# Performance work log

Measured on AMD Instinct MI355X. Metric: run time of the kernel, lower is better.

The kernel has to match this reference:

```python
import jax, jax.numpy as jnp
import numpy as np

EPS = 1e-5


def setup_inputs() -> dict:
    key = jax.random.key(0)
    ks = jax.random.split(key, 12)
    B, C, D, H, W = 16, 32, 32, 64, 64
    HID, OUT = 256, 128
    inp = {
        "x": jax.random.normal(ks[0], (B, C, D, H, W), dtype=jnp.float32),
        "bn_gamma": jax.random.normal(ks[1], (C,), dtype=jnp.float32) * 0.1 + 1.0,
        "bn_beta": jax.random.normal(ks[2], (C,), dtype=jnp.float32) * 0.1,
        "w_ih": jax.random.normal(ks[3], (HID, C), dtype=jnp.float32) / np.sqrt(C),
        "b_ih": jax.random.normal(ks[4], (HID,), dtype=jnp.float32) * 0.01,
        "w_hh": jax.random.normal(ks[5], (HID, HID), dtype=jnp.float32) / np.sqrt(HID),
        "b_hh": jax.random.normal(ks[6], (HID,), dtype=jnp.float32) * 0.01,
        "w_out": jax.random.normal(ks[7], (OUT, HID), dtype=jnp.float32) / np.sqrt(HID),
        "b_out": jax.random.normal(ks[8], (OUT,), dtype=jnp.float32) * 0.01,
        "ln_gamma": jnp.ones((OUT,), dtype=jnp.float32),
        "ln_beta": jnp.zeros((OUT,), dtype=jnp.float32),
        "pooled_depth": 8,
    }
    return inp


def reference(x, bn_gamma, bn_beta, w_ih, b_ih, w_hh, b_hh, w_out, b_out, ln_gamma, ln_beta, pooled_depth):
    B, C, D, H, W = x.shape
    P = pooled_depth
    # SyncBatchNorm (training mode: batch statistics over B, D, H, W per channel)
    mean = jnp.mean(x, axis=(0, 2, 3, 4), keepdims=True)
    var = jnp.mean((x - mean) ** 2, axis=(0, 2, 3, 4), keepdims=True)  # biased var
    g = bn_gamma.reshape(1, C, 1, 1, 1)
    b = bn_beta.reshape(1, C, 1, 1, 1)
    x = (x - mean) * jax.lax.rsqrt(var + EPS) * g + b
    x = jax.nn.relu(x)
    # AdaptiveMaxPool3d -> (P, 1, 1); D divisible by P so bins are uniform
    x = x.reshape(B, C, P, D // P, H, W).max(axis=(3, 4, 5))  # (B, C, P)
    x = jnp.transpose(x, (2, 0, 1))  # (P, B, C) -- time-major
    # RNNCell (relu) scan over time
    hx0 = jnp.zeros((B, w_hh.shape[0]), dtype=x.dtype)

    def step(hx, xt):
        hx = jax.nn.relu(xt @ w_ih.T + b_ih + hx @ w_hh.T + b_hh)
        return hx, None

    hx, _ = jax.lax.scan(step, hx0, x)
    # Output projection + LayerNorm
    out = hx @ w_out.T + b_out  # (B, OUT)
    mu = jnp.mean(out, axis=-1, keepdims=True)
    v = jnp.mean((out - mu) ** 2, axis=-1, keepdims=True)
    out = (out - mu) * jax.lax.rsqrt(v + EPS) * ln_gamma + ln_beta
    return out
```

## Files before the change

### kernel.cpp

```cpp
#include <hip/hip_runtime.h>
#include <math.h>

#define EPS 1e-5f

constexpr int Bc = 16, Cc = 32, Dc = 32, Hc = 64, Wc = 64;
constexpr int Pc = 8, HIDc = 256, OUTc = 128;
constexpr int NBINS = Bc * Cc * Pc;
constexpr float NPC_INV = 1.0f / (float)(Bc * Dc * Hc * Wc);


__global__ __launch_bounds__(256) void k1_stats(const float* __restrict__ x,
                                                float* __restrict__ ws) {
    const int bid = blockIdx.x;
    const int t = threadIdx.x;
    const float4* px = reinterpret_cast<const float4*>(x) + ((size_t)bid << 12);

    float vmax = -INFINITY, vmin = INFINITY, s = 0.f, ss = 0.f;
#pragma unroll
    for (int j = 0; j < 16; ++j) {
        float4 v = px[j * 256 + t];
        vmax = fmaxf(vmax, fmaxf(fmaxf(v.x, v.y), fmaxf(v.z, v.w)));
        vmin = fminf(vmin, fminf(fminf(v.x, v.y), fminf(v.z, v.w)));
        s += (v.x + v.y) + (v.z + v.w);
        ss = fmaf(v.x, v.x, ss); ss = fmaf(v.y, v.y, ss);
        ss = fmaf(v.z, v.z, ss); ss = fmaf(v.w, v.w, ss);
    }
#pragma unroll
    for (int off = 1; off < 64; off <<= 1) {
        vmax = fmaxf(vmax, __shfl_xor(vmax, off));
        vmin = fminf(vmin, __shfl_xor(vmin, off));
        s += __shfl_xor(s, off);
        ss += __shfl_xor(ss, off);
    }
    __shared__ float r[4][4];
    const int wid = t >> 6;
    if ((t & 63) == 0) { r[wid][0] = vmax; r[wid][1] = vmin; r[wid][2] = s; r[wid][3] = ss; }
    __syncthreads();
    if (t == 0) {
        vmax = fmaxf(fmaxf(r[0][0], r[1][0]), fmaxf(r[2][0], r[3][0]));
        vmin = fminf(fminf(r[0][1], r[1][1]), fminf(r[2][1], r[3][1]));
        s  = (r[0][2] + r[1][2]) + (r[2][2] + r[3][2]);
        ss = (r[0][3] + r[1][3]) + (r[2][3] + r[3][3]);
        ws[bid]             = vmax;
        ws[NBINS + bid]     = vmin;
        ws[2 * NBINS + bid] = s;
        ws[3 * NBINS + bid] = ss;
    }
}

__global__ __launch_bounds__(256) void k2_rnn(const float* __restrict__ ws,
                                              const float* __restrict__ bn_gamma,
                                              const float* __restrict__ bn_beta,
                                              const float* __restrict__ w_ih,
                                              const float* __restrict__ b_ih,
                                              const float* __restrict__ w_hh,
                                              const float* __restrict__ b_hh,
                                              const float* __restrict__ w_out,
                                              const float* __restrict__ b_out,
                                              const float* __restrict__ ln_gamma,
                                              const float* __restrict__ ln_beta,
                                              float* __restrict__ out) {
    const int b = blockIdx.x;
    const int t = threadIdx.x;

    __shared__ float scale_s[Cc], shift_s[Cc];
    __shared__ __align__(16) float pooled[Pc][Cc];
    __shared__ __align__(16) float u[Pc][HIDc];
    __shared__ __align__(16) float hx[2][HIDc];
    __shared__ __align__(16) float o[OUTc];
    __shared__ float red2[2];

    {
        const int c = t >> 3, r = t & 7;
        float s = 0.f, ss = 0.f;
        for (int j = 0; j < 16; ++j) {
            const int i = r + 8 * j;
            const int bid = ((i >> 3) * Cc + c) * Pc + (i & 7);
            s  += ws[2 * NBINS + bid];
            ss += ws[3 * NBINS + bid];
        }
#pragma unroll
        for (int off = 1; off < 8; off <<= 1) {
            s  += __shfl_xor(s, off);
            ss += __shfl_xor(ss, off);
        }
        if (r == 0) {
            const float mean = s * NPC_INV;
            const float var  = ss * NPC_INV - mean * mean;
            const float sc   = bn_gamma[c] * rsqrtf(var + EPS);
            scale_s[c] = sc;
            shift_s[c] = bn_beta[c] - mean * sc;
        }
    }
    __syncthreads();

    {
        const int p = t >> 5, c = t & 31;
        const int bid = (b * Cc + c) * Pc + p;
        const float sc = scale_s[c];
        const float xm = (sc >= 0.f) ? ws[bid] : ws[NBINS + bid];
        pooled[p][c] = fmaxf(fmaf(sc, xm, shift_s[c]), 0.f);
    }
    __syncthreads();

    {
        const float4* wi = reinterpret_cast<const float4*>(w_ih) + t * (Cc / 4);
        float4 wiv[8];
#pragma unroll
        for (int q = 0; q < 8; ++q) wiv[q] = wi[q];
        const float bias = b_ih[t] + b_hh[t];
#pragma unroll
        for (int p = 0; p < Pc; ++p) {
            const float4* pl = reinterpret_cast<const float4*>(&pooled[p][0]);
            float a0 = bias, a1 = 0.f, a2 = 0.f, a3 = 0.f;
#pragma unroll
            for (int q = 0; q < 8; ++q) {
                float4 pv = pl[q];
                a0 = fmaf(pv.x, wiv[q].x, a0);
                a1 = fmaf(pv.y, wiv[q].y, a1);
                a2 = fmaf(pv.z, wiv[q].z, a2);
                a3 = fmaf(pv.w, wiv[q].w, a3);
            }
            u[p][t] = (a0 + a1) + (a2 + a3);
        }
        hx[0][t] = fmaxf(u[0][t], 0.f);
    }
    __syncthreads();

    int cur = 0;
    const float4* wrow = reinterpret_cast<const float4*>(w_hh) + t * (HIDc / 4);
    for (int step = 1; step < Pc; ++step) {
        const float4* hv4 = reinterpret_cast<const float4*>(&hx[cur][0]);
        float a0 = u[step][t], a1 = 0.f, a2 = 0.f, a3 = 0.f;
#pragma unroll
        for (int k4 = 0; k4 < HIDc / 4; ++k4) {
            float4 wv = wrow[k4];
            float4 hv = hv4[k4];
            a0 = fmaf(hv.x, wv.x, a0);
            a1 = fmaf(hv.y, wv.y, a1);
            a2 = fmaf(hv.z, wv.z, a2);
            a3 = fmaf(hv.w, wv.w, a3);
        }
        hx[cur ^ 1][t] = fmaxf((a0 + a1) + (a2 + a3), 0.f);
        __syncthreads();
        cur ^= 1;
    }

    if (t < OUTc) {
        const float4* wo = reinterpret_cast<const float4*>(w_out) + t * (HIDc / 4);
        const float4* hv4 = reinterpret_cast<const float4*>(&hx[cur][0]);
        float a0 = b_out[t], a1 = 0.f, a2 = 0.f, a3 = 0.f;
#pragma unroll
        for (int k4 = 0; k4 < HIDc / 4; ++k4) {
            float4 wv = wo[k4];
            float4 hv = hv4[k4];
            a0 = fmaf(hv.x, wv.x, a0);
            a1 = fmaf(hv.y, wv.y, a1);
            a2 = fmaf(hv.z, wv.z, a2);
            a3 = fmaf(hv.w, wv.w, a3);
        }
        o[t] = (a0 + a1) + (a2 + a3);
    }
    __syncthreads();
    if (t < 64) {
        const float x0 = o[t], x1 = o[t + 64];
        float s = x0 + x1, ss = x0 * x0 + x1 * x1;
#pragma unroll
        for (int off = 1; off < 64; off <<= 1) {
            s  += __shfl_xor(s, off);
            ss += __shfl_xor(ss, off);
        }
        if (t == 0) { red2[0] = s; red2[1] = ss; }
    }
    __syncthreads();
    if (t < OUTc) {
        const float mu  = red2[0] * (1.0f / OUTc);
        const float var = red2[1] * (1.0f / OUTc) - mu * mu;
        const float rs  = rsqrtf(var + EPS);
        out[b * OUTc + t] = (o[t] - mu) * rs * ln_gamma[t] + ln_beta[t];
    }
}

extern "C" void kernel_launch(void* const* d_in, const int* in_sizes, int n_in,
                              void* d_out, int out_size, void* d_ws, size_t ws_size,
                              hipStream_t stream) {
    const float* x        = (const float*)d_in[0];
    const float* bn_gamma = (const float*)d_in[1];
    const float* bn_beta  = (const float*)d_in[2];
    const float* w_ih     = (const float*)d_in[3];
    const float* b_ih     = (const float*)d_in[4];
    const float* w_hh     = (const float*)d_in[5];
    const float* b_hh     = (const float*)d_in[6];
    const float* w_out    = (const float*)d_in[7];
    const float* b_out    = (const float*)d_in[8];
    const float* ln_gamma = (const float*)d_in[9];
    const float* ln_beta  = (const float*)d_in[10];
    float* out = (float*)d_out;
    float* ws  = (float*)d_ws;

    k1_stats<<<NBINS, 256, 0, stream>>>(x, ws);
    k2_rnn<<<Bc, 256, 0, stream>>>(ws, bn_gamma, bn_beta, w_ih, b_ih, w_hh, b_hh,
                                   w_out, b_out, ln_gamma, ln_beta, out);
}
```

Before: 68.71 us.

## Split RNN recurrence across 1024 threads with register-resident w_hh slices

The RNN kernel grows from 256 to 1024 threads per batch block. Each hidden unit's dot product is split into four K-segments whose partial sums are reduced through shared memory, and each thread keeps its w_hh slice in registers across all timesteps. The output projection is likewise split four ways with a shuffle reduction, and the BN stat reduction uses wider lanes. This shortens the serial latency of the small second kernel but adds an extra barrier per step and more register pressure, while the dominant stats kernel is unchanged.

```diff
diff --git a/kernel.cpp b/kernel.cpp
--- a/kernel.cpp
+++ b/kernel.cpp
@@ -48,39 +48,43 @@
     }
 }
 
-__global__ __launch_bounds__(256) void k2_rnn(const float* __restrict__ ws,
-                                              const float* __restrict__ bn_gamma,
-                                              const float* __restrict__ bn_beta,
-                                              const float* __restrict__ w_ih,
-                                              const float* __restrict__ b_ih,
-                                              const float* __restrict__ w_hh,
-                                              const float* __restrict__ b_hh,
-                                              const float* __restrict__ w_out,
-                                              const float* __restrict__ b_out,
-                                              const float* __restrict__ ln_gamma,
-                                              const float* __restrict__ ln_beta,
-                                              float* __restrict__ out) {
+__global__ __launch_bounds__(1024) void k2_rnn(const float* __restrict__ ws,
+                                               const float* __restrict__ bn_gamma,
+                                               const float* __restrict__ bn_beta,
+                                               const float* __restrict__ w_ih,
+                                               const float* __restrict__ b_ih,
+                                               const float* __restrict__ w_hh,
+                                               const float* __restrict__ b_hh,
+                                               const float* __restrict__ w_out,
+                                               const float* __restrict__ b_out,
+                                               const float* __restrict__ ln_gamma,
+                                               const float* __restrict__ ln_beta,
+                                               float* __restrict__ out) {
     const int b = blockIdx.x;
     const int t = threadIdx.x;
+    const int h = t & 255;
+    const int q = t >> 8;
 
     __shared__ float scale_s[Cc], shift_s[Cc];
     __shared__ __align__(16) float pooled[Pc][Cc];
     __shared__ __align__(16) float u[Pc][HIDc];
-    __shared__ __align__(16) float hx[2][HIDc];
+    __shared__ __align__(16) float hx[HIDc];
+    __shared__ __align__(16) float part[4][HIDc];
     __shared__ __align__(16) float o[OUTc];
     __shared__ float red2[2];
 
     {
-        const int c = t >> 3, r = t & 7;
+        const int c = t >> 5, r = t & 31;
         float s = 0.f, ss = 0.f;
-        for (int j = 0; j < 16; ++j) {
-            const int i = r + 8 * j;
+#pragma unroll
+        for (int j = 0; j < 4; ++j) {
+            const int i = r + 32 * j;
             const int bid = ((i >> 3) * Cc + c) * Pc + (i & 7);
             s  += ws[2 * NBINS + bid];
             ss += ws[3 * NBINS + bid];
         }
 #pragma unroll
-        for (int off = 1; off < 8; off <<= 1) {
+        for (int off = 1; off < 32; off <<= 1) {
             s  += __shfl_xor(s, off);
             ss += __shfl_xor(ss, off);
         }
@@ -94,7 +98,7 @@
     }
     __syncthreads();
 
-    {
+    if (t < Pc * Cc) {
         const int p = t >> 5, c = t & 31;
         const int bid = (b * Cc + c) * Pc + p;
         const float sc = scale_s[c];
@@ -104,64 +108,81 @@
     __syncthreads();
 
     {
-        const float4* wi = reinterpret_cast<const float4*>(w_ih) + t * (Cc / 4);
+        const float4* wi = reinterpret_cast<const float4*>(w_ih) + h * (Cc / 4);
         float4 wiv[8];
 #pragma unroll
-        for (int q = 0; q < 8; ++q) wiv[q] = wi[q];
-        const float bias = b_ih[t] + b_hh[t];
-#pragma unroll
-        for (int p = 0; p < Pc; ++p) {
+        for (int e = 0; e < 8; ++e) wiv[e] = wi[e];
+        const float bias = b_ih[h] + b_hh[h];
+#pragma unroll
+        for (int pp = 0; pp < 2; ++pp) {
+            const int p = q + 4 * pp;
             const float4* pl = reinterpret_cast<const float4*>(&pooled[p][0]);
             float a0 = bias, a1 = 0.f, a2 = 0.f, a3 = 0.f;
 #pragma unroll
-            for (int q = 0; q < 8; ++q) {
-                float4 pv = pl[q];
-                a0 = fmaf(pv.x, wiv[q].x, a0);
-                a1 = fmaf(pv.y, wiv[q].y, a1);
-                a2 = fmaf(pv.z, wiv[q].z, a2);
-                a3 = fmaf(pv.w, wiv[q].w, a3);
+            for (int e = 0; e < 8; ++e) {
+                float4 pv = pl[e];
+                a0 = fmaf(pv.x, wiv[e].x, a0);
+                a1 = fmaf(pv.y, wiv[e].y, a1);
+                a2 = fmaf(pv.z, wiv[e].z, a2);
+                a3 = fmaf(pv.w, wiv[e].w, a3);
             }
-            u[p][t] = (a0 + a1) + (a2 + a3);
-        }
-        hx[0][t] = fmaxf(u[0][t], 0.f);
-    }
-    __syncthreads();
-
-    int cur = 0;
-    const float4* wrow = reinterpret_cast<const float4*>(w_hh) + t * (HIDc / 4);
+            u[p][h] = (a0 + a1) + (a2 + a3);
+        }
+    }
+
+    float4 wreg[16];
+    {
+        const float4* wr = reinterpret_cast<const float4*>(w_hh) + h * (HIDc / 4) + q * 16;
+#pragma unroll
+        for (int e = 0; e < 16; ++e) wreg[e] = wr[e];
+    }
+    __syncthreads();
+
+    if (t < HIDc) hx[t] = fmaxf(u[0][t], 0.f);
+    __syncthreads();
+
     for (int step = 1; step < Pc; ++step) {
-        const float4* hv4 = reinterpret_cast<const float4*>(&hx[cur][0]);
-        float a0 = u[step][t], a1 = 0.f, a2 = 0.f, a3 = 0.f;
-#pragma unroll
-        for (int k4 = 0; k4 < HIDc / 4; ++k4) {
-            float4 wv = wrow[k4];
-            float4 hv = hv4[k4];
+        const float4* hv4 = reinterpret_cast<const float4*>(&hx[q * 64]);
+        float a0 = 0.f, a1 = 0.f, a2 = 0.f, a3 = 0.f;
+#pragma unroll
+        for (int e = 0; e < 16; ++e) {
+            float4 wv = wreg[e];
+            float4 hv = hv4[e];
             a0 = fmaf(hv.x, wv.x, a0);
             a1 = fmaf(hv.y, wv.y, a1);
             a2 = fmaf(hv.z, wv.z, a2);
             a3 = fmaf(hv.w, wv.w, a3);
         }
-        hx[cur ^ 1][t] = fmaxf((a0 + a1) + (a2 + a3), 0.f);
+        part[q][h] = (a0 + a1) + (a2 + a3);
         __syncthreads();
-        cur ^= 1;
-    }
-
-    if (t < OUTc) {
-        const float4* wo = reinterpret_cast<const float4*>(w_out) + t * (HIDc / 4);
-        const float4* hv4 = reinterpret_cast<const float4*>(&hx[cur][0]);
-        float a0 = b_out[t], a1 = 0.f, a2 = 0.f, a3 = 0.f;
-#pragma unroll
-        for (int k4 = 0; k4 < HIDc / 4; ++k4) {
-            float4 wv = wo[k4];
-            float4 hv = hv4[k4];
+        if (q == 0) {
+            const float v = u[step][h] + ((part[0][h] + part[1][h]) + (part[2][h] + part[3][h]));
+            hx[h] = fmaxf(v, 0.f);
+        }
+        __syncthreads();
+    }
+
+    if (t < 4 * OUTc) {
+        const int oi = t >> 2, seg = t & 3;
+        const float4* wo = reinterpret_cast<const float4*>(w_out) + oi * (HIDc / 4) + seg * 16;
+        const float4* hv4 = reinterpret_cast<const float4*>(&hx[seg * 64]);
+        float a0 = (seg == 0) ? b_out[oi] : 0.f, a1 = 0.f, a2 = 0.f, a3 = 0.f;
+#pragma unroll
+        for (int e = 0; e < 16; ++e) {
+            float4 wv = wo[e];
+            float4 hv = hv4[e];
             a0 = fmaf(hv.x, wv.x, a0);
             a1 = fmaf(hv.y, wv.y, a1);
             a2 = fmaf(hv.z, wv.z, a2);
             a3 = fmaf(hv.w, wv.w, a3);
         }
-        o[t] = (a0 + a1) + (a2 + a3);
-    }
-    __syncthreads();
+        float s = (a0 + a1) + (a2 + a3);
+        s += __shfl_xor(s, 1);
+        s += __shfl_xor(s, 2);
+        if (seg == 0) o[oi] = s;
+    }
+    __syncthreads();
+
     if (t < 64) {
         const float x0 = o[t], x1 = o[t + 64];
         float s = x0 + x1, ss = x0 * x0 + x1 * x1;
@@ -199,6 +220,6 @@
     float* ws  = (float*)d_ws;
 
     k1_stats<<<NBINS, 256, 0, stream>>>(x, ws);
-    k2_rnn<<<Bc, 256, 0, stream>>>(ws, bn_gamma, bn_beta, w_ih, b_ih, w_hh, b_hh,
-                                   w_out, b_out, ln_gamma, ln_beta, out);
+    k2_rnn<<<Bc, 1024, 0, stream>>>(ws, bn_gamma, bn_beta, w_ih, b_ih, w_hh, b_hh,
+                                    w_out, b_out, ln_gamma, ln_beta, out);
 }
```

Result: faster. 66.07 us (-3.8%).
